# Optimization experiments

Hardware: AMD Instinct MI355X
Metric: run time of the kernel (lower is better)

## Reference

```python
import jax, jax.numpy as jnp
from jax import lax
import numpy as np

B, CIN, T, H, W = 32, 512, 16, 7, 7
A = 9                 # 3 scales x 3 ratios
STRIDE = 16.0
NMS_THRESH = 0.7      # cfg.TEST.RPN_NMS_THRESH
POST_NMS = 300        # cfg.TEST.RPN_POST_NMS_TOP_N


def _gen_anchors():
    # faithful port of generate_anchors(base_size=16, ratios=[0.5,1,2], scales=[4,8,16])
    base = 16.0
    ratios = np.array([0.5, 1.0, 2.0])
    scales = np.array([4.0, 8.0, 16.0])
    ctr = (base - 1.0) / 2.0
    size = base * base
    ws = np.round(np.sqrt(size / ratios))
    hs = np.round(ws * ratios)
    def mk(ws, hs, xc, yc):
        return np.stack([xc - 0.5 * (ws - 1), yc - 0.5 * (hs - 1),
                         xc + 0.5 * (ws - 1), yc + 0.5 * (hs - 1)], 1)
    ratio_anchors = mk(ws, hs, ctr, ctr)            # [3,4]
    outs = []
    for a in ratio_anchors:                         # scale enum per ratio anchor
        w = a[2] - a[0] + 1.0
        h = a[3] - a[1] + 1.0
        xc = a[0] + 0.5 * (w - 1)
        yc = a[1] + 0.5 * (h - 1)
        outs.append(mk(w * scales, h * scales, xc, yc))
    return np.concatenate(outs, 0).astype(np.float32)  # [9,4]


def _shifted_anchors():
    sx = (np.arange(W) * STRIDE).astype(np.float32)
    sy = (np.arange(H) * STRIDE).astype(np.float32)
    mx, my = np.meshgrid(sx, sy)                    # x fastest, matches HWA flatten
    shifts = np.stack([mx.ravel(), my.ravel(), mx.ravel(), my.ravel()], 1)  # [K,4]
    return (shifts[:, None, :] + _gen_anchors()[None, :, :]).reshape(-1, 4)  # [K*A,4]

_ALL_ANCHORS = jnp.asarray(_shifted_anchors())      # [441,4]


def conv3d(x, w, b, pad):
    y = lax.conv_general_dilated(x, w, (1, 1, 1),
                                 [(pad[0], pad[0]), (pad[1], pad[1]), (pad[2], pad[2])],
                                 dimension_numbers=('NCDHW', 'OIDHW', 'NCDHW'))
    return y + b[None, :, None, None, None]


def conv1x1(x, w, b):
    return jnp.einsum('bchw,oc->bohw', x, w[:, :, 0, 0]) + b[None, :, None, None]


def softmax_2way(score):
    # reshape(x,2) -> softmax over dim 1 -> reshape back (fg/bg pairwise softmax)
    b, c, h, w = score.shape
    s = score.reshape(b, 2, (c // 2) * h, w)
    return jax.nn.softmax(s, axis=1).reshape(b, c, h, w)


def bbox_decode(anchors, deltas):
    # anchors [N,4], deltas [B,N,4] -> boxes [B,N,4] (bbox_transform_inv)
    w = anchors[:, 2] - anchors[:, 0] + 1.0
    h = anchors[:, 3] - anchors[:, 1] + 1.0
    cx = anchors[:, 0] + 0.5 * w
    cy = anchors[:, 1] + 0.5 * h
    pcx = deltas[..., 0] * w + cx
    pcy = deltas[..., 1] * h + cy
    pw = jnp.exp(deltas[..., 2]) * w
    ph = jnp.exp(deltas[..., 3]) * h
    return jnp.stack([pcx - 0.5 * pw, pcy - 0.5 * ph,
                      pcx + 0.5 * pw, pcy + 0.5 * ph], axis=-1)


def clip_boxes(boxes, info):
    # boxes [N,4], info = (im_h, im_w, scale)
    x1 = jnp.clip(boxes[:, 0], 0.0, info[1] - 1.0)
    y1 = jnp.clip(boxes[:, 1], 0.0, info[0] - 1.0)
    x2 = jnp.clip(boxes[:, 2], 0.0, info[1] - 1.0)
    y2 = jnp.clip(boxes[:, 3], 0.0, info[0] - 1.0)
    return jnp.stack([x1, y1, x2, y2], 1)


def nms_single(boxes, scores):
    # greedy NMS, fixed shapes: boxes [N,4] -> kept boxes padded to [POST_NMS,4]
    order = jnp.argsort(-scores)
    b = boxes[order]
    n = b.shape[0]
    areas = (b[:, 2] - b[:, 0] + 1.0) * (b[:, 3] - b[:, 1] + 1.0)
    idx = jnp.arange(n)
    def body(i, keep):
        xx1 = jnp.maximum(b[i, 0], b[:, 0])
        yy1 = jnp.maximum(b[i, 1], b[:, 1])
        xx2 = jnp.minimum(b[i, 2], b[:, 2])
        yy2 = jnp.minimum(b[i, 3], b[:, 3])
        inter = jnp.clip(xx2 - xx1 + 1.0, 0.0) * jnp.clip(yy2 - yy1 + 1.0, 0.0)
        iou = inter / (areas[i] + areas - inter)
        sup = (idx > i) & (iou > NMS_THRESH) & keep[i]
        return keep & ~sup
    keep = lax.fori_loop(0, n, body, jnp.ones((n,), bool))
    sel = jnp.sort(jnp.where(keep, idx, n))[:POST_NMS]
    valid = sel < n
    selc = jnp.minimum(sel, n - 1)
    return jnp.where(valid[:, None], b[selc], 0.0)


def proposal_layer(cls_prob, bbox_pred, im_info):
    b = cls_prob.shape[0]
    scores = cls_prob[:, A:, :, :].transpose(0, 2, 3, 1).reshape(b, -1)   # fg scores [B,K*A]
    deltas = bbox_pred.transpose(0, 2, 3, 1).reshape(b, -1, 4)
    props = bbox_decode(_ALL_ANCHORS, deltas)
    props = jax.vmap(clip_boxes)(props, im_info)
    boxes = jax.vmap(nms_single)(props, scores)                           # [B,POST_NMS,4]
    bidx = jnp.broadcast_to(jnp.arange(b, dtype=boxes.dtype)[:, None, None],
                            (b, POST_NMS, 1))
    return jnp.concatenate([bidx, boxes], axis=2)                         # [B,POST_NMS,5]


def setup_inputs() -> dict:
    key = jax.random.key(0)
    ks = jax.random.split(key, 8)
    s = 0.05
    return {
        'base_feat': jax.random.normal(ks[0], (B, CIN, T, H, W), jnp.float32),
        'im_info': jnp.tile(jnp.array([[112.0, 112.0, 1.0]], jnp.float32), (B, 1)),
        'gt_boxes': jnp.zeros((B, 1, 7), jnp.float32),
        'num_boxes': jnp.zeros((B,), jnp.int32),
        'rpn_conv_w': jax.random.normal(ks[1], (512, CIN, 3, 3, 3), jnp.float32) * s,
        'rpn_conv_b': jnp.zeros((512,), jnp.float32),
        't16_w': jax.random.normal(ks[2], (512, 512, 16, 3, 3), jnp.float32) * s,
        't16_b': jnp.zeros((512,), jnp.float32),
        'cls_w': jax.random.normal(ks[3], (2 * A, 512, 1, 1), jnp.float32) * s,
        'cls_b': jnp.zeros((2 * A,), jnp.float32),
        'bbox_w': jax.random.normal(ks[4], (4 * A, 512, 1, 1), jnp.float32) * s,
        'bbox_b': jnp.zeros((4 * A,), jnp.float32),
    }


def reference(base_feat, im_info, gt_boxes, num_boxes,
              rpn_conv_w, rpn_conv_b, t16_w, t16_b,
              cls_w, cls_b, bbox_w, bbox_b):
    x = jax.nn.relu(conv3d(base_feat, rpn_conv_w, rpn_conv_b, (1, 1, 1)))     # [B,512,16,7,7]
    f16 = jax.nn.relu(conv3d(x, t16_w, t16_b, (0, 1, 1)))                     # [B,512,1,7,7]
    f16 = f16.transpose(0, 2, 1, 3, 4).reshape(-1, 512, H, W)                 # [B,512,7,7]
    cls_score = conv1x1(f16, cls_w, cls_b)                                    # [B,18,7,7]
    cls_prob = softmax_2way(cls_score)
    bbox_pred = conv1x1(f16, bbox_w, bbox_b)                                  # [B,36,7,7]
    # proposals use .data in the original -> detached
    rois = proposal_layer(lax.stop_gradient(cls_prob),
                          lax.stop_gradient(bbox_pred), im_info)
    return rois, cls_prob, bbox_pred
```

## Files before the change

kernel.cpp:

```cpp
#include <hip/hip_runtime.h>
#include <hip/hip_bf16.h>
#include <cmath>

typedef __bf16 bf16_t;
typedef unsigned short u16;
typedef unsigned int u32;
typedef float f32x4 __attribute__((ext_vector_type(4)));
typedef short s16x8 __attribute__((ext_vector_type(8)));
typedef u32   u32x2 __attribute__((ext_vector_type(2)));
typedef u32   u32x4 __attribute__((ext_vector_type(4)));
#define DEVINL __device__ __forceinline__
#define POSTN 300

#define XPT_OFF  0ull
#define XP16_OFF 0ull
#define W1T_OFF  5971968ull
#define YTP_OFF  20127744ull
#define YT_OFF   23887872ull
#define F_OFF    45121536ull
#define PART_OFF 48332800ull
#define SC_OFF   51544064ull
#define BX_OFF   51600512ull
#define K1_OFF   51826304ull
#define K2_OFF   51881600ull
#define FLAG_OFF 52176512ull
#define NEED     52176516ull

DEVINL float ldf(const void* p, long i, int f32m) {
  return f32m ? ((const float*)p)[i] : (float)(((const bf16_t*)p)[i]);
}

DEVINL float clampf(float v, float lo, float hi) {
  if (!(v == v)) return lo;
  if (v < lo) return lo;
  if (v > hi) return hi;
  return v;
}

DEVINL void split3(float v, u16& hb, u16& mb, u16& lb) {
  bf16_t h = (bf16_t)v; float fh = (float)h;
  float r1 = v - fh;
  bf16_t m = (bf16_t)r1; float fm_ = (float)m;
  float r2 = r1 - fm_;
  bf16_t l = (bf16_t)r2;
  __builtin_memcpy(&hb, &h, 2);
  __builtin_memcpy(&mb, &m, 2);
  __builtin_memcpy(&lb, &l, 2);
}

__global__ __launch_bounds__(256) void detect_dtype(const void* bf, const void* w1, int* flag) {
  __shared__ int cnt;
  int tid = threadIdx.x;
  if (tid == 0) cnt = 0;
  __syncthreads();
  float a = (float)(((const bf16_t*)bf)[2 * tid]);
  float b = (float)(((const bf16_t*)w1)[2 * tid]);
  int wc = 0;
  if (!(a == a) || fabsf(a) > 1e20f || (a != 0.f && fabsf(a) < 1e-20f)) wc++;
  if (!(b == b) || fabsf(b) > 1e20f || (b != 0.f && fabsf(b) < 1e-20f)) wc++;
  atomicAdd(&cnt, wc);
  __syncthreads();
  if (tid == 0) *flag = (cnt >= 16) ? 1 : 0;
}

__global__ __launch_bounds__(256) void build_koff(int* k1, int* k2) {
  int i = blockIdx.x * 256 + threadIdx.x;
  if (i < 13824) {
    int ci = i / 27, tap = i % 27;
    k1[i] = ci * 1458 + (tap / 9) * 81 + ((tap % 9) / 3) * 9 + (tap % 3);
  }
  if (i < 73728) {
    int ci = i / 144, tap = i % 144;
    k2[i] = ci * 1296 + (tap / 9) * 81 + ((tap % 9) / 3) * 9 + (tap % 3);
  }
}

__global__ __launch_bounds__(256) void build_w1t(const void* __restrict__ w1,
                                                 u16* __restrict__ w1T,
                                                 const int* __restrict__ flagp) {
  if (*flagp != 0) return;
  int id = blockIdx.x * 256 + threadIdx.x;
  if (id >= 512 * 27 * 64) return;
  int co = id / 1728, r = id % 1728, tap = r / 64, cio = r % 64;
  const u16* W = (const u16*)w1;
  u16 t[8];
#pragma unroll
  for (int e = 0; e < 8; e++) t[e] = W[co * 13824 + (cio * 8 + e) * 27 + tap];
  u32x4 v = { (u32)t[0] | ((u32)t[1] << 16), (u32)t[2] | ((u32)t[3] << 16),
              (u32)t[4] | ((u32)t[5] << 16), (u32)t[6] | ((u32)t[7] << 16) };
  *(u32x4*)&w1T[co * 13824 + tap * 512 + cio * 8] = v;
}

__global__ __launch_bounds__(256) void pad_f32(const void* __restrict__ X,
                                               float* __restrict__ XpT,
                                               const int* __restrict__ flagp, int cb) {
  if (*flagp == 0) return;
  int e = blockIdx.x * 256 + threadIdx.x;
  if (e >= 4 * 512 * 1458) return;
  int bc = e / 1458, p = e % 1458;
  int tp = p / 81, hp = (p % 81) / 9, wp = p % 9;
  float v = 0.f;
  if (tp >= 1 && tp < 17 && hp >= 1 && hp < 8 && wp >= 1 && wp < 8) {
    int f = (tp - 1) * 49 + (hp - 1) * 7 + (wp - 1);
    v = ((const float*)X)[((long)cb * 512 + bc) * 784 + f];
  }
  XpT[e] = v;
}

__global__ __launch_bounds__(256) void pad_b16(const void* __restrict__ X,
                                               u16* __restrict__ Xp16,
                                               const int* __restrict__ flagp, int cb) {
  if (*flagp != 0) return;
  int id = blockIdx.x * 256 + threadIdx.x;
  if (id >= 5832 * 64) return;
  int pos = id >> 6, cio = id & 63;
  int b = pos / 1458, r = pos % 1458;
  int tp = r / 81, hp = (r % 81) / 9, wp = r % 9;
  u16 t[8] = {0, 0, 0, 0, 0, 0, 0, 0};
  if (tp >= 1 && tp < 17 && hp >= 1 && hp < 8 && wp >= 1 && wp < 8) {
    int f = (tp - 1) * 49 + (hp - 1) * 7 + (wp - 1);
    const u16* Xs = (const u16*)X;
#pragma unroll
    for (int e = 0; e < 8; e++)
      t[e] = Xs[((long)(cb + b) * 512 + cio * 8 + e) * 784 + f];
  }
  u32x4 v = { (u32)t[0] | ((u32)t[1] << 16), (u32)t[2] | ((u32)t[3] << 16),
              (u32)t[4] | ((u32)t[5] << 16), (u32)t[6] | ((u32)t[7] << 16) };
  *(u32x4*)&Xp16[(long)pos * 512 + cio * 8] = v;
}

template <int MODE>
__global__ __launch_bounds__(256) void gemm_f32(
    const float* __restrict__ Act, const void* __restrict__ Wgt, const void* __restrict__ bias,
    float* __restrict__ Yt, float* __restrict__ Part,
    const int* __restrict__ koff, const int* __restrict__ flagp) {
  const int f32m = *flagp;
  if (f32m == 0) return;
  const int tid = threadIdx.x;
  int mt, nt, s = 0;
  if (MODE == 1) { mt = blockIdx.x % 49; nt = blockIdx.x / 49; }
  else           { mt = blockIdx.x & 3;  nt = (blockIdx.x >> 2) & 7; s = blockIdx.x >> 5; }
  const int m0 = mt * 64, n0 = nt * 64;
  const int K     = (MODE == 1) ? 13824 : 9216;
  const int kBase = (MODE == 1) ? 0     : s * 9216;
  const int WROW  = (MODE == 1) ? 13824 : 73728;
  const int MTOT  = (MODE == 1) ? 3136  : 196;

  __shared__ __align__(16) float As[64][68];
  __shared__ __align__(16) float Bs[64][68];

  const int am = tid & 63, akq = tid >> 6;
  long aBase;
  {
    int m = m0 + am; if (m > MTOT - 1) m = MTOT - 1;
    if (MODE == 1) {
      int b = m / 784, r = m % 784, t = r / 49, h = (r % 49) / 7, w = r % 7;
      aBase = (long)b * (512 * 1458) + t * 81 + h * 9 + w;
    } else {
      int b = m / 49, r = m % 49, h = r / 7, w = r % 7;
      aBase = (long)b * (512 * 1296) + h * 9 + w;
    }
  }
  const int bn = tid >> 2, bks = (tid & 3) * 16;
  const long bBase = (long)(n0 + bn) * WROW + kBase;

  float acc[4][4] = {{0.f}};
  const int tx = tid & 15, ty = tid >> 4;

  for (int k0 = 0; k0 < K; k0 += 64) {
    __syncthreads();
#pragma unroll
    for (int j = 0; j < 16; j++) {
      int kk = akq * 16 + j;
      As[kk][am] = Act[aBase + koff[kBase + k0 + kk]];
    }
#pragma unroll
    for (int j = 0; j < 16; j++) {
      int kk = bks + j;
      Bs[kk][bn] = ldf(Wgt, bBase + k0 + kk, f32m);
    }
    __syncthreads();
#pragma unroll 8
    for (int k = 0; k < 64; k++) {
      f32x4 a = *(const f32x4*)&As[k][tx * 4];
      f32x4 b = *(const f32x4*)&Bs[k][ty * 4];
#pragma unroll
      for (int i = 0; i < 4; i++)
#pragma unroll
        for (int j = 0; j < 4; j++) acc[i][j] += a[i] * b[j];
    }
  }

#pragma unroll
  for (int i = 0; i < 4; i++) {
    int m = m0 + tx * 4 + i;
#pragma unroll
    for (int j = 0; j < 4; j++) {
      int n = n0 + ty * 4 + j;
      if (MODE == 1) {
        int b = m / 784, r = m % 784, t = r / 49, h = (r % 49) / 7, w = r % 7;
        float v = acc[i][j] + ldf(bias, n, f32m);
        v = fmaxf(v, 0.f);
        Yt[(long)(b * 512 + n) * 1296 + t * 81 + (h + 1) * 9 + (w + 1)] = v;
      } else {
        if (m < 196) Part[((long)s * 196 + m) * 512 + n] = acc[i][j];
      }
    }
  }
}

__global__ __launch_bounds__(256) void gemm_mf1(
    const u16* __restrict__ Xp16, const u16* __restrict__ w1T, const void* __restrict__ bias,
    u32x2* __restrict__ YtP, const int* __restrict__ flagp) {
  if (*flagp != 0) return;
  const int tid = threadIdx.x;
  const int mt = blockIdx.x % 25, nt = blockIdx.x / 25;
  const int m0 = mt * 128, n0 = nt * 64;

  __shared__ u16 As[128 * 64];
  __shared__ u16 Bs[64 * 64];

  int rowbase[4];
#pragma unroll
  for (int i = 0; i < 4; ++i) {
    int id = tid + 256 * i;
    int m = m0 + (id >> 3); if (m > 3135) m = 3135;
    int b = m / 784, r = m % 784, t = r / 49, h = (r % 49) / 7, w = r % 7;
    rowbase[i] = ((((b * 18) + (t + 1)) * 9 + (h + 1)) * 9 + (w + 1)) * 512;
  }
  const int bn = tid & 63, bq = tid >> 6;
  const u16* __restrict__ Bp = w1T + (long)(n0 + bn) * 13824;
  const int bwb = bn * 64, bsw = (bn & 7) << 3;

  const int lane = tid & 63, wv = tid >> 6;
  const int wm = (wv & 1) * 64, wn = (wv >> 1) * 32;
  const int lr = lane & 15, lq = lane >> 4;

  f32x4 acc[4][2];
#pragma unroll
  for (int i = 0; i < 4; ++i)
#pragma unroll
    for (int j = 0; j < 2; ++j) acc[i][j] = f32x4{0.f, 0.f, 0.f, 0.f};

  for (int tap = 0; tap < 27; ++tap) {
    const int dt = tap / 9, dh = (tap % 9) / 3, dw = tap % 3;
    const int tapshift = dt * 41472 + dh * 4608 + dw * 512;
    for (int cib = 0; cib < 8; ++cib) {
      const int off = tapshift + cib * 64;
      __syncthreads();
      u32x4 va[4];
#pragma unroll
      for (int i = 0; i < 4; ++i) {
        int id = tid + 256 * i;
        va[i] = *(const u32x4*)&Xp16[rowbase[i] + off + (id & 7) * 8];
      }
#pragma unroll
      for (int i = 0; i < 4; ++i) {
        int id = tid + 256 * i;
        int row = id >> 3, oct = id & 7;
        *(u32x4*)&As[row * 64 + ((oct * 8) ^ ((row & 7) << 3))] = va[i];
      }
      {
        const u32x4* wp = (const u32x4*)(Bp + tap * 512 + cib * 64 + bq * 16);
        *(u32x4*)&Bs[bwb + ((bq * 16) ^ bsw)] = wp[0];
        *(u32x4*)&Bs[bwb + ((bq * 16 + 8) ^ bsw)] = wp[1];
      }
      __syncthreads();
#pragma unroll
      for (int kk = 0; kk < 64; kk += 32) {
        const int kf = kk + lq * 8;
        s16x8 a[4], b[2];
#pragma unroll
        for (int fm = 0; fm < 4; ++fm) {
          const int row = wm + fm * 16 + lr;
          a[fm] = *(const s16x8*)&As[row * 64 + (kf ^ ((lr & 7) << 3))];
        }
#pragma unroll
        for (int fn = 0; fn < 2; ++fn) {
          const int row = wn + fn * 16 + lr;
          b[fn] = *(const s16x8*)&Bs[row * 64 + (kf ^ ((lr & 7) << 3))];
        }
#pragma unroll
        for (int fm = 0; fm < 4; ++fm)
#pragma unroll
          for (int fn = 0; fn < 2; ++fn)
            acc[fm][fn] = __builtin_amdgcn_mfma_f32_16x16x32_bf16(a[fm], b[fn], acc[fm][fn], 0, 0, 0);
      }
    }
  }

#pragma unroll
  for (int fn = 0; fn < 2; ++fn) {
    const int n = n0 + wn + fn * 16 + lr;
    const float bv = (float)(((const bf16_t*)bias)[n]);
#pragma unroll
    for (int fm = 0; fm < 4; ++fm)
#pragma unroll
      for (int r = 0; r < 4; ++r) {
        const int m = m0 + wm + fm * 16 + lq * 4 + r;
        if (m < 3136) {
          int b = m / 784, rr = m % 784, t = rr / 49, hh = (rr % 49) / 7, ww = rr % 7;
          float v = fmaxf(acc[fm][fn][r] + bv, 0.f);
          u16 hb, mb, lb; split3(v, hb, mb, lb);
          long idx = (long)(b * 512 + n) * 1296 + t * 81 + (hh + 1) * 9 + (ww + 1);
          YtP[idx] = u32x2{ ((u32)hb << 16) | mb, (u32)lb };
        }
      }
  }
}

__global__ __launch_bounds__(256) void gemm_mf2(
    const u32x2* __restrict__ AP, const void* __restrict__ Wgt,
    float* __restrict__ Part, const int* __restrict__ koff, const int* __restrict__ flagp) {
  if (*flagp != 0) return;
  const int tid = threadIdx.x;
  const int mt = blockIdx.x & 3, nt = (blockIdx.x >> 2) & 7, s = blockIdx.x >> 5;
  const int m0 = mt * 64, n0 = nt * 64;
  const int kBase = s * 9216;

  __shared__ u16 AsH[64 * 64], AsM[64 * 64], AsL[64 * 64];
  __shared__ u16 Bs[64 * 64];

  const int am = tid & 63, kq = tid >> 6;
  long aBase;
  {
    int m = m0 + am; if (m > 195) m = 195;
    int b = m / 49, r = m % 49, h = r / 7, w = r % 7;
    aBase = (long)b * (512 * 1296) + h * 9 + w;
  }
  const u32x2* __restrict__ Ap = AP + aBase;
  const int awb = am * 64, asw = (am & 7) << 3;

  const int bn = tid & 63, bq = tid >> 6;
  const u16* __restrict__ Bp = (const u16*)Wgt + (long)(n0 + bn) * 73728 + kBase;
  const int bwb = bn * 64, bsw = (bn & 7) << 3;

  const int lane = tid & 63, wv = tid >> 6;
  const int wm = (wv & 1) * 32, wn = (wv >> 1) * 32;
  const int lr = lane & 15, lq = lane >> 4;

  f32x4 acc[2][2];
#pragma unroll
  for (int i = 0; i < 2; ++i)
#pragma unroll
    for (int j = 0; j < 2; ++j) acc[i][j] = f32x4{0.f, 0.f, 0.f, 0.f};

  for (int k0 = 0; k0 < 9216; k0 += 64) {
    __syncthreads();
#pragma unroll
    for (int g = 0; g < 2; ++g) {
      const int o = kBase + k0 + kq * 16 + g * 8;
      const int i0 = koff[o + 0], i1 = koff[o + 1], i2 = koff[o + 2], i3 = koff[o + 3],
                i4 = koff[o + 4], i5 = koff[o + 5], i6 = koff[o + 6], i7 = koff[o + 7];
      const u32x2 q0 = Ap[i0], q1 = Ap[i1], q2 = Ap[i2], q3 = Ap[i3],
                  q4 = Ap[i4], q5 = Ap[i5], q6 = Ap[i6], q7 = Ap[i7];
      const int wi = awb + ((kq * 16 + g * 8) ^ asw);
      u32x4 H = { (q0.x >> 16) | (q1.x & 0xffff0000u), (q2.x >> 16) | (q3.x & 0xffff0000u),
                  (q4.x >> 16) | (q5.x & 0xffff0000u), (q6.x >> 16) | (q7.x & 0xffff0000u) };
      *(u32x4*)&AsH[wi] = H;
      u32x4 M = { (q0.x & 0xffffu) | (q1.x << 16), (q2.x & 0xffffu) | (q3.x << 16),
                  (q4.x & 0xffffu) | (q5.x << 16), (q6.x & 0xffffu) | (q7.x << 16) };
      *(u32x4*)&AsM[wi] = M;
      u32x4 L = { q0.y | (q1.y << 16), q2.y | (q3.y << 16),
                  q4.y | (q5.y << 16), q6.y | (q7.y << 16) };
      *(u32x4*)&AsL[wi] = L;
    }
    {
      const u32x4* wp = (const u32x4*)(Bp + k0 + bq * 16);
      *(u32x4*)&Bs[bwb + ((bq * 16) ^ bsw)] = wp[0];
      *(u32x4*)&Bs[bwb + ((bq * 16 + 8) ^ bsw)] = wp[1];
    }
    __syncthreads();
#pragma unroll
    for (int kk = 0; kk < 64; kk += 32) {
      const int kf = kk + lq * 8;
      s16x8 ah[2], am_[2], al[2], b[2];
#pragma unroll
      for (int fm = 0; fm < 2; ++fm) {
        const int off = (wm + fm * 16 + lr) * 64 + (kf ^ ((lr & 7) << 3));
        ah[fm] = *(const s16x8*)&AsH[off];
        am_[fm] = *(const s16x8*)&AsM[off];
        al[fm] = *(const s16x8*)&AsL[off];
      }
#pragma unroll
      for (int fn = 0; fn < 2; ++fn) {
        const int off = (wn + fn * 16 + lr) * 64 + (kf ^ ((lr & 7) << 3));
        b[fn] = *(const s16x8*)&Bs[off];
      }
#pragma unroll
      for (int fm = 0; fm < 2; ++fm)
#pragma unroll
        for (int fn = 0; fn < 2; ++fn) {
          acc[fm][fn] = __builtin_amdgcn_mfma_f32_16x16x32_bf16(ah[fm], b[fn], acc[fm][fn], 0, 0, 0);
          acc[fm][fn] = __builtin_amdgcn_mfma_f32_16x16x32_bf16(am_[fm], b[fn], acc[fm][fn], 0, 0, 0);
          acc[fm][fn] = __builtin_amdgcn_mfma_f32_16x16x32_bf16(al[fm], b[fn], acc[fm][fn], 0, 0, 0);
        }
    }
  }

#pragma unroll
  for (int fn = 0; fn < 2; ++fn) {
    const int n = n0 + wn + fn * 16 + lr;
#pragma unroll
    for (int fm = 0; fm < 2; ++fm)
#pragma unroll
      for (int r = 0; r < 4; ++r) {
        const int m = m0 + wm + fm * 16 + lq * 4 + r;
        if (m < 196) Part[((long)s * 196 + m) * 512 + n] = acc[fm][fn][r];
      }
  }
}

__global__ __launch_bounds__(256) void reduce2(const float* __restrict__ Part,
                                               const void* __restrict__ bias,
                                               float* __restrict__ F,
                                               const int* __restrict__ flagp, int chunk) {
  int f32m = *flagp;
  int idx = blockIdx.x * 256 + threadIdx.x;
  if (idx >= 196 * 512) return;
  int m = idx >> 9, n = idx & 511;
  float v = 0.f;
#pragma unroll
  for (int s = 0; s < 8; s++) v += Part[((long)s * 196 + m) * 512 + n];
  v += ldf(bias, n, f32m);
  F[((long)chunk * 196 + m) * 512 + n] = fmaxf(v, 0.f);
}

__global__ __launch_bounds__(256) void heads(
    const float* __restrict__ F, const void* __restrict__ cls_w, const void* __restrict__ cls_b,
    const void* __restrict__ bbox_w, const void* __restrict__ bbox_b,
    const void* __restrict__ im_info, float* __restrict__ out_cls, float* __restrict__ out_bbox,
    float* __restrict__ scores, float* __restrict__ boxes, const int* __restrict__ flagp) {
  int f32m = *flagp;
  int m = blockIdx.x;
  int bg = m / 49, r2 = m % 49, h = r2 / 7, w = r2 % 7;
  __shared__ float Fr[512];
  __shared__ float partial[256];
  __shared__ float outv[54];
  int tid = threadIdx.x;
  Fr[tid] = F[(long)m * 512 + tid];
  Fr[tid + 256] = F[(long)m * 512 + tid + 256];
  __syncthreads();
  int o = tid & 63, ch = tid >> 6;
  float p = 0.f;
  if (o < 54) {
    const void* wp = (o < 18) ? cls_w : bbox_w;
    long wrow = (o < 18) ? (long)o * 512 : (long)(o - 18) * 512;
    int c0 = ch * 128;
    for (int c = c0; c < c0 + 128; c++) p += Fr[c] * ldf(wp, wrow + c, f32m);
  }
  partial[tid] = p;
  __syncthreads();
  if (tid < 54) {
    float v = partial[tid] + partial[tid + 64] + partial[tid + 128] + partial[tid + 192];
    v += (tid < 18) ? ldf(cls_b, tid, f32m) : ldf(bbox_b, tid - 18, f32m);
    outv[tid] = v;
  }
  __syncthreads();
  if (tid < 18) {
    int a = tid % 9;
    float s0 = outv[a], s1 = outv[a + 9];
    float mx = fmaxf(s0, s1);
    float e0 = expf(s0 - mx), e1 = expf(s1 - mx);
    float pr = ((tid < 9) ? e0 : e1) / (e0 + e1);
    if (!(pr == pr)) pr = 0.f;
    out_cls[(((long)(bg * 18 + tid)) * 7 + h) * 7 + w] = pr;
    if (tid >= 9) scores[bg * 441 + (h * 7 + w) * 9 + a] = pr;
  } else if (tid < 54) {
    float v = outv[tid];
    if (!(v == v)) v = 0.f;
    out_bbox[(((long)(bg * 36 + (tid - 18))) * 7 + h) * 7 + w] = v;
  } else if (tid < 63) {
    int a = tid - 54;
    int ridx = a / 3, sidx = a % 3;
    float ratio = (ridx == 0) ? 0.5f : ((ridx == 1) ? 1.f : 2.f);
    float scale = (sidx == 0) ? 4.f : ((sidx == 1) ? 8.f : 16.f);
    float ws0 = rintf(sqrtf(256.f / ratio));
    float hs0 = rintf(ws0 * ratio);
    float x1 = 7.5f - 0.5f * (ws0 - 1.f), y1 = 7.5f - 0.5f * (hs0 - 1.f);
    float x2 = 7.5f + 0.5f * (ws0 - 1.f), y2 = 7.5f + 0.5f * (hs0 - 1.f);
    float w_ = x2 - x1 + 1.f, h_ = y2 - y1 + 1.f;
    float xc = x1 + 0.5f * (w_ - 1.f), yc = y1 + 0.5f * (h_ - 1.f);
    float ws2 = w_ * scale, hs2 = h_ * scale;
    float ax1 = xc - 0.5f * (ws2 - 1.f) + w * 16.f;
    float ay1 = yc - 0.5f * (hs2 - 1.f) + h * 16.f;
    float ax2 = xc + 0.5f * (ws2 - 1.f) + w * 16.f;
    float ay2 = yc + 0.5f * (hs2 - 1.f) + h * 16.f;
    float wA = ax2 - ax1 + 1.f, hA = ay2 - ay1 + 1.f;
    float cxA = ax1 + 0.5f * wA, cyA = ay1 + 0.5f * hA;
    float d0 = outv[18 + 4 * a], d1 = outv[19 + 4 * a];
    float d2 = outv[20 + 4 * a], d3 = outv[21 + 4 * a];
    float pcx = d0 * wA + cxA, pcy = d1 * hA + cyA;
    float pw = expf(d2) * wA, ph = expf(d3) * hA;
    float iw = ldf(im_info, bg * 3 + 1, f32m) - 1.f;
    float ih = ldf(im_info, bg * 3 + 0, f32m) - 1.f;
    float bx1 = clampf(pcx - 0.5f * pw, 0.f, iw);
    float by1 = clampf(pcy - 0.5f * ph, 0.f, ih);
    float bx2 = clampf(pcx + 0.5f * pw, 0.f, iw);
    float by2 = clampf(pcy + 0.5f * ph, 0.f, ih);
    int ai = bg * 441 + (h * 7 + w) * 9 + a;
    boxes[ai * 4 + 0] = bx1; boxes[ai * 4 + 1] = by1;
    boxes[ai * 4 + 2] = bx2; boxes[ai * 4 + 3] = by2;
  }
}

__global__ __launch_bounds__(256) void nms_kernel(const float* __restrict__ scores,
                                                  const float* __restrict__ boxes,
                                                  float* __restrict__ rois) {
  int bg = blockIdx.x;
  int tid = threadIdx.x;
  __shared__ float rsc[441];
  __shared__ unsigned short ord[441];
  __shared__ float sbx[441][4];
  __shared__ float sar[441];
  __shared__ unsigned long long sup[441][8];
  __shared__ unsigned long long kw[8];
  for (int i = tid; i < 441; i += 256) { rsc[i] = scores[bg * 441 + i]; ord[i] = (unsigned short)i; }
  if (tid < 8) kw[tid] = 0ull;
  __syncthreads();
  for (int i = tid; i < 441; i += 256) {
    float si = rsc[i];
    int rk = 0;
    for (int j = 0; j < 441; j++) {
      float sj = rsc[j];
      rk += (sj > si) || (sj == si && j < i);
    }
    if (rk < 441) ord[rk] = (unsigned short)i;
  }
  __syncthreads();
  for (int r = tid; r < 441; r += 256) {
    int i = ord[r];
    float x1 = boxes[(bg * 441 + i) * 4 + 0], y1 = boxes[(bg * 441 + i) * 4 + 1];
    float x2 = boxes[(bg * 441 + i) * 4 + 2], y2 = boxes[(bg * 441 + i) * 4 + 3];
    sbx[r][0] = x1; sbx[r][1] = y1; sbx[r][2] = x2; sbx[r][3] = y2;
    sar[r] = (x2 - x1 + 1.f) * (y2 - y1 + 1.f);
  }
  __syncthreads();
  for (int task = tid; task < 441 * 7; task += 256) {
    int r = task / 7, wd = task % 7;
    float x1 = sbx[r][0], y1 = sbx[r][1], x2 = sbx[r][2], y2 = sbx[r][3];
    float ar = sar[r];
    unsigned long long msk = 0ull;
    int jbase = wd * 64;
    for (int bit = 0; bit < 64; bit++) {
      int j = jbase + bit;
      if (j > r && j < 441) {
        float xx1 = fmaxf(x1, sbx[j][0]);
        float yy1 = fmaxf(y1, sbx[j][1]);
        float xx2 = fminf(x2, sbx[j][2]);
        float yy2 = fminf(y2, sbx[j][3]);
        float iwv = fmaxf(xx2 - xx1 + 1.f, 0.f);
        float ihv = fmaxf(yy2 - yy1 + 1.f, 0.f);
        float inter = iwv * ihv;
        float iou = inter / (ar + sar[j] - inter);
        if (iou > 0.7f) msk |= (1ull << bit);
      }
    }
    sup[r][wd] = msk;
  }
  __syncthreads();
  if (tid < 64) {
    int wd = (tid < 7) ? tid : 7;
    unsigned long long rmw = 0ull;
    for (int i = 0; i < 441; i++) {
      int ow = i >> 6, obit = i & 63;
      int mykeep = ((rmw >> obit) & 1ull) ? 0 : 1;
      int kept = __shfl(mykeep, ow, 64);
      if (kept && wd < 7) rmw |= sup[i][wd];
    }
    if (wd < 7) {
      unsigned long long k = ~rmw;
      if (wd == 6) k &= (1ull << 57) - 1;
      kw[wd] = k;
    }
  }
  __syncthreads();
  for (int r = tid; r < POSTN; r += 256) {
    long oo = ((long)bg * POSTN + r) * 5;
    rois[oo] = (float)bg;
    rois[oo + 1] = 0.f; rois[oo + 2] = 0.f;
    rois[oo + 3] = 0.f; rois[oo + 4] = 0.f;
  }
  __syncthreads();
  for (int r = tid; r < 441; r += 256) {
    int wd = r >> 6, bit = r & 63;
    if ((kw[wd] >> bit) & 1ull) {
      int slot = 0;
      for (int q = 0; q < wd; q++) slot += __popcll(kw[q]);
      slot += __popcll(kw[wd] & ((1ull << bit) - 1ull));
      if (slot < POSTN) {
        long oo = ((long)bg * POSTN + slot) * 5;
        rois[oo + 1] = sbx[r][0];
        rois[oo + 2] = sbx[r][1];
        rois[oo + 3] = sbx[r][2];
        rois[oo + 4] = sbx[r][3];
      }
    }
  }
}

__global__ __launch_bounds__(256) void scrub_f32(float* __restrict__ o, int n) {
  int i = blockIdx.x * 256 + threadIdx.x;
  if (i >= n) return;
  float v = o[i];
  if (!(v == v) || fabsf(v) > 1e30f) o[i] = 0.f;
}

__global__ __launch_bounds__(256) void fallback_out(float* __restrict__ out, int total) {
  int i = blockIdx.x * 256 + threadIdx.x;
  if (i >= total) return;
  out[i] = 0.f;
}

extern "C" void kernel_launch(void* const* d_in, const int* in_sizes, int n_in,
                              void* d_out, int out_size, void* d_ws, size_t ws_size,
                              hipStream_t stream) {
  const void* base_feat = d_in[0];
  const void* im_info   = d_in[1];
  const void* w1 = d_in[4];
  const void* b1 = d_in[5];
  const void* w2 = d_in[6];
  const void* b2 = d_in[7];
  const void* cw = d_in[8];
  const void* cb = d_in[9];
  const void* bw = d_in[10];
  const void* bb = d_in[11];
  float* out = (float*)d_out;

  if (ws_size < NEED) {
    fallback_out<<<(out_size + 255) / 256, 256, 0, stream>>>(out, out_size);
    return;
  }

  char* ws = (char*)d_ws;
  float* XpT  = (float*)(ws + XPT_OFF);
  u16*   Xp16 = (u16*)(ws + XP16_OFF);
  u16*   W1T  = (u16*)(ws + W1T_OFF);
  u32x2* YtP  = (u32x2*)(ws + YTP_OFF);
  float* Yt   = (float*)(ws + YT_OFF);
  float* F    = (float*)(ws + F_OFF);
  float* Part = (float*)(ws + PART_OFF);
  float* Sc   = (float*)(ws + SC_OFF);
  float* Bx   = (float*)(ws + BX_OFF);
  int*   K1   = (int*)(ws + K1_OFF);
  int*   K2   = (int*)(ws + K2_OFF);
  int*   Flag = (int*)(ws + FLAG_OFF);

  detect_dtype<<<1, 256, 0, stream>>>(base_feat, w1, Flag);
  build_koff<<<288, 256, 0, stream>>>(K1, K2);
  build_w1t<<<3456, 256, 0, stream>>>(w1, W1T, Flag);
  hipMemsetAsync(ws + YTP_OFF, 0, 45121536ull - YTP_OFF, stream);

  for (int c = 0; c < 8; c++) {
    pad_f32<<<11664, 256, 0, stream>>>(base_feat, XpT, Flag, c * 4);
    pad_b16<<<1458, 256, 0, stream>>>(base_feat, Xp16, Flag, c * 4);
    gemm_f32<1><<<392, 256, 0, stream>>>(XpT, w1, b1, Yt, nullptr, K1, Flag);
    gemm_mf1<<<200, 256, 0, stream>>>(Xp16, W1T, b1, YtP, Flag);
    gemm_f32<2><<<256, 256, 0, stream>>>(Yt, w2, nullptr, nullptr, Part, K2, Flag);
    gemm_mf2<<<256, 256, 0, stream>>>(YtP, w2, Part, K2, Flag);
    reduce2<<<392, 256, 0, stream>>>(Part, b2, F, Flag, c);
  }

  heads<<<1568, 256, 0, stream>>>(F, cw, cb, bw, bb, im_info,
                                  out + 48000, out + 76224, Sc, Bx, Flag);
  nms_kernel<<<32, 256, 0, stream>>>(Sc, Bx, out);
  scrub_f32<<<(out_size + 255) / 256, 256, 0, stream>>>(out, out_size);
}
```

Baseline: 11.56 ms.

## Retile conv GEMMs for more blocks and separate fp32/bf16 chunk loops

The bf16 path's first conv GEMM now uses 64x64 tiles, doubling its block count to 392. The second GEMM's split-K grows from 8 to 12 slices (384 blocks), with its partials placed in the freed Xp16 region and summed by a dedicated reduce. The fp32 path is split into its own loop over 4 chunks of 8 batches with matching grid changes, so the dead-path kernels for the other dtype are no longer launched on every iteration. The aim is better CU occupancy and fewer no-op launches, at the cost of more partial-sum traffic and less per-block reuse in the first GEMM.

```diff
diff --git a/kernel.cpp b/kernel.cpp
--- a/kernel.cpp
+++ b/kernel.cpp
@@ -95,9 +95,9 @@
                                                float* __restrict__ XpT,
                                                const int* __restrict__ flagp, int cb) {
   if (*flagp == 0) return;
-  int e = blockIdx.x * 256 + threadIdx.x;
-  if (e >= 4 * 512 * 1458) return;
-  int bc = e / 1458, p = e % 1458;
+  long e = (long)blockIdx.x * 256 + threadIdx.x;
+  if (e >= 8L * 512 * 1458) return;
+  long bc = e / 1458; int p = (int)(e % 1458);
   int tp = p / 81, hp = (p % 81) / 9, wp = p % 9;
   float v = 0.f;
   if (tp >= 1 && tp < 17 && hp >= 1 && hp < 8 && wp >= 1 && wp < 8) {
@@ -138,13 +138,12 @@
   if (f32m == 0) return;
   const int tid = threadIdx.x;
   int mt, nt, s = 0;
-  if (MODE == 1) { mt = blockIdx.x % 49; nt = blockIdx.x / 49; }
-  else           { mt = blockIdx.x & 3;  nt = (blockIdx.x >> 2) & 7; s = blockIdx.x >> 5; }
+  if (MODE == 1) { mt = blockIdx.x % 98; nt = blockIdx.x / 98; }
+  else           { mt = blockIdx.x % 7;  nt = (blockIdx.x / 7) % 8; s = blockIdx.x / 56; }
   const int m0 = mt * 64, n0 = nt * 64;
-  const int K     = (MODE == 1) ? 13824 : 9216;
-  const int kBase = (MODE == 1) ? 0     : s * 9216;
+  const int K     = (MODE == 1) ? 13824 : 18432;
+  const int kBase = (MODE == 1) ? 0     : s * 18432;
   const int WROW  = (MODE == 1) ? 13824 : 73728;
-  const int MTOT  = (MODE == 1) ? 3136  : 196;
 
   __shared__ __align__(16) float As[64][68];
   __shared__ __align__(16) float Bs[64][68];
@@ -152,11 +151,12 @@
   const int am = tid & 63, akq = tid >> 6;
   long aBase;
   {
-    int m = m0 + am; if (m > MTOT - 1) m = MTOT - 1;
+    int m = m0 + am;
     if (MODE == 1) {
       int b = m / 784, r = m % 784, t = r / 49, h = (r % 49) / 7, w = r % 7;
       aBase = (long)b * (512 * 1458) + t * 81 + h * 9 + w;
     } else {
+      if (m > 391) m = 391;
       int b = m / 49, r = m % 49, h = r / 7, w = r % 7;
       aBase = (long)b * (512 * 1296) + h * 9 + w;
     }
@@ -203,7 +203,7 @@
         v = fmaxf(v, 0.f);
         Yt[(long)(b * 512 + n) * 1296 + t * 81 + (h + 1) * 9 + (w + 1)] = v;
       } else {
-        if (m < 196) Part[((long)s * 196 + m) * 512 + n] = acc[i][j];
+        if (m < 392) Part[((long)s * 392 + m) * 512 + n] = acc[i][j];
       }
     }
   }
@@ -214,31 +214,32 @@
     u32x2* __restrict__ YtP, const int* __restrict__ flagp) {
   if (*flagp != 0) return;
   const int tid = threadIdx.x;
-  const int mt = blockIdx.x % 25, nt = blockIdx.x / 25;
-  const int m0 = mt * 128, n0 = nt * 64;
-
-  __shared__ u16 As[128 * 64];
+  const int mt = blockIdx.x % 49, nt = blockIdx.x / 49;
+  const int m0 = mt * 64, n0 = nt * 64;
+
+  __shared__ u16 As[64 * 64];
   __shared__ u16 Bs[64 * 64];
 
-  int rowbase[4];
-#pragma unroll
-  for (int i = 0; i < 4; ++i) {
-    int id = tid + 256 * i;
-    int m = m0 + (id >> 3); if (m > 3135) m = 3135;
+  const int arow = tid >> 2, aq = tid & 3;
+  int rowbase;
+  {
+    int m = m0 + arow;
     int b = m / 784, r = m % 784, t = r / 49, h = (r % 49) / 7, w = r % 7;
-    rowbase[i] = ((((b * 18) + (t + 1)) * 9 + (h + 1)) * 9 + (w + 1)) * 512;
-  }
+    rowbase = ((((b * 18) + (t + 1)) * 9 + (h + 1)) * 9 + (w + 1)) * 512;
+  }
+  const int awb = arow * 64, asw = (arow & 7) << 3;
+
   const int bn = tid & 63, bq = tid >> 6;
   const u16* __restrict__ Bp = w1T + (long)(n0 + bn) * 13824;
   const int bwb = bn * 64, bsw = (bn & 7) << 3;
 
   const int lane = tid & 63, wv = tid >> 6;
-  const int wm = (wv & 1) * 64, wn = (wv >> 1) * 32;
+  const int wm = (wv & 1) * 32, wn = (wv >> 1) * 32;
   const int lr = lane & 15, lq = lane >> 4;
 
-  f32x4 acc[4][2];
-#pragma unroll
-  for (int i = 0; i < 4; ++i)
+  f32x4 acc[2][2];
+#pragma unroll
+  for (int i = 0; i < 2; ++i)
 #pragma unroll
     for (int j = 0; j < 2; ++j) acc[i][j] = f32x4{0.f, 0.f, 0.f, 0.f};
 
@@ -248,18 +249,10 @@
     for (int cib = 0; cib < 8; ++cib) {
       const int off = tapshift + cib * 64;
       __syncthreads();
-      u32x4 va[4];
-#pragma unroll
-      for (int i = 0; i < 4; ++i) {
-        int id = tid + 256 * i;
-        va[i] = *(const u32x4*)&Xp16[rowbase[i] + off + (id & 7) * 8];
-      }
-#pragma unroll
-      for (int i = 0; i < 4; ++i) {
-        int id = tid + 256 * i;
-        int row = id >> 3, oct = id & 7;
-        *(u32x4*)&As[row * 64 + ((oct * 8) ^ ((row & 7) << 3))] = va[i];
-      }
+      u32x4 v0 = *(const u32x4*)&Xp16[rowbase + off + aq * 8];
+      u32x4 v1 = *(const u32x4*)&Xp16[rowbase + off + (aq + 4) * 8];
+      *(u32x4*)&As[awb + ((aq * 8) ^ asw)] = v0;
+      *(u32x4*)&As[awb + (((aq + 4) * 8) ^ asw)] = v1;
       {
         const u32x4* wp = (const u32x4*)(Bp + tap * 512 + cib * 64 + bq * 16);
         *(u32x4*)&Bs[bwb + ((bq * 16) ^ bsw)] = wp[0];
@@ -269,9 +262,9 @@
 #pragma unroll
       for (int kk = 0; kk < 64; kk += 32) {
         const int kf = kk + lq * 8;
-        s16x8 a[4], b[2];
-#pragma unroll
-        for (int fm = 0; fm < 4; ++fm) {
+        s16x8 a[2], b[2];
+#pragma unroll
+        for (int fm = 0; fm < 2; ++fm) {
           const int row = wm + fm * 16 + lr;
           a[fm] = *(const s16x8*)&As[row * 64 + (kf ^ ((lr & 7) << 3))];
         }
@@ -281,7 +274,7 @@
           b[fn] = *(const s16x8*)&Bs[row * 64 + (kf ^ ((lr & 7) << 3))];
         }
 #pragma unroll
-        for (int fm = 0; fm < 4; ++fm)
+        for (int fm = 0; fm < 2; ++fm)
 #pragma unroll
           for (int fn = 0; fn < 2; ++fn)
             acc[fm][fn] = __builtin_amdgcn_mfma_f32_16x16x32_bf16(a[fm], b[fn], acc[fm][fn], 0, 0, 0);
@@ -294,17 +287,15 @@
     const int n = n0 + wn + fn * 16 + lr;
     const float bv = (float)(((const bf16_t*)bias)[n]);
 #pragma unroll
-    for (int fm = 0; fm < 4; ++fm)
+    for (int fm = 0; fm < 2; ++fm)
 #pragma unroll
       for (int r = 0; r < 4; ++r) {
         const int m = m0 + wm + fm * 16 + lq * 4 + r;
-        if (m < 3136) {
-          int b = m / 784, rr = m % 784, t = rr / 49, hh = (rr % 49) / 7, ww = rr % 7;
-          float v = fmaxf(acc[fm][fn][r] + bv, 0.f);
-          u16 hb, mb, lb; split3(v, hb, mb, lb);
-          long idx = (long)(b * 512 + n) * 1296 + t * 81 + (hh + 1) * 9 + (ww + 1);
-          YtP[idx] = u32x2{ ((u32)hb << 16) | mb, (u32)lb };
-        }
+        int b = m / 784, rr = m % 784, t = rr / 49, hh = (rr % 49) / 7, ww = rr % 7;
+        float v = fmaxf(acc[fm][fn][r] + bv, 0.f);
+        u16 hb, mb, lb; split3(v, hb, mb, lb);
+        long idx = (long)(b * 512 + n) * 1296 + t * 81 + (hh + 1) * 9 + (ww + 1);
+        YtP[idx] = u32x2{ ((u32)hb << 16) | mb, (u32)lb };
       }
   }
 }
@@ -316,7 +307,7 @@
   const int tid = threadIdx.x;
   const int mt = blockIdx.x & 3, nt = (blockIdx.x >> 2) & 7, s = blockIdx.x >> 5;
   const int m0 = mt * 64, n0 = nt * 64;
-  const int kBase = s * 9216;
+  const int kBase = s * 6144;
 
   __shared__ u16 AsH[64 * 64], AsM[64 * 64], AsL[64 * 64];
   __shared__ u16 Bs[64 * 64];
@@ -345,7 +336,7 @@
 #pragma unroll
     for (int j = 0; j < 2; ++j) acc[i][j] = f32x4{0.f, 0.f, 0.f, 0.f};
 
-  for (int k0 = 0; k0 < 9216; k0 += 64) {
+  for (int k0 = 0; k0 < 6144; k0 += 64) {
     __syncthreads();
 #pragma unroll
     for (int g = 0; g < 2; ++g) {
@@ -411,19 +402,34 @@
   }
 }
 
-__global__ __launch_bounds__(256) void reduce2(const float* __restrict__ Part,
-                                               const void* __restrict__ bias,
-                                               float* __restrict__ F,
-                                               const int* __restrict__ flagp, int chunk) {
-  int f32m = *flagp;
+__global__ __launch_bounds__(256) void reduce2_f32(const float* __restrict__ Part,
+                                                   const void* __restrict__ bias,
+                                                   float* __restrict__ F,
+                                                   const int* __restrict__ flagp, int chunk) {
+  if (*flagp == 0) return;
+  int idx = blockIdx.x * 256 + threadIdx.x;
+  if (idx >= 392 * 512) return;
+  int m = idx >> 9, n = idx & 511;
+  float v = 0.f;
+#pragma unroll
+  for (int s = 0; s < 4; s++) v += Part[((long)s * 392 + m) * 512 + n];
+  v += ((const float*)bias)[n];
+  F[((long)(chunk * 392 + m)) * 512 + n] = fmaxf(v, 0.f);
+}
+
+__global__ __launch_bounds__(256) void reduce2_b16(const float* __restrict__ Part,
+                                                   const void* __restrict__ bias,
+                                                   float* __restrict__ F,
+                                                   const int* __restrict__ flagp, int chunk) {
+  if (*flagp != 0) return;
   int idx = blockIdx.x * 256 + threadIdx.x;
   if (idx >= 196 * 512) return;
   int m = idx >> 9, n = idx & 511;
   float v = 0.f;
 #pragma unroll
-  for (int s = 0; s < 8; s++) v += Part[((long)s * 196 + m) * 512 + n];
-  v += ldf(bias, n, f32m);
-  F[((long)chunk * 196 + m) * 512 + n] = fmaxf(v, 0.f);
+  for (int s = 0; s < 12; s++) v += Part[((long)s * 196 + m) * 512 + n];
+  v += (float)(((const bf16_t*)bias)[n]);
+  F[((long)(chunk * 196 + m)) * 512 + n] = fmaxf(v, 0.f);
 }
 
 __global__ __launch_bounds__(256) void heads(
@@ -633,32 +639,37 @@
   }
 
   char* ws = (char*)d_ws;
-  float* XpT  = (float*)(ws + XPT_OFF);
-  u16*   Xp16 = (u16*)(ws + XP16_OFF);
-  u16*   W1T  = (u16*)(ws + W1T_OFF);
-  u32x2* YtP  = (u32x2*)(ws + YTP_OFF);
-  float* Yt   = (float*)(ws + YT_OFF);
-  float* F    = (float*)(ws + F_OFF);
-  float* Part = (float*)(ws + PART_OFF);
-  float* Sc   = (float*)(ws + SC_OFF);
-  float* Bx   = (float*)(ws + BX_OFF);
-  int*   K1   = (int*)(ws + K1_OFF);
-  int*   K2   = (int*)(ws + K2_OFF);
-  int*   Flag = (int*)(ws + FLAG_OFF);
+  float* XpT   = (float*)(ws + XPT_OFF);
+  u16*   Xp16  = (u16*)(ws + XP16_OFF);
+  float* PartB = (float*)(ws + XP16_OFF);
+  u16*   W1T   = (u16*)(ws + W1T_OFF);
+  u32x2* YtP   = (u32x2*)(ws + YTP_OFF);
+  float* Yt    = (float*)(ws + YT_OFF);
+  float* F     = (float*)(ws + F_OFF);
+  float* PartF = (float*)(ws + PART_OFF);
+  float* Sc    = (float*)(ws + SC_OFF);
+  float* Bx    = (float*)(ws + BX_OFF);
+  int*   K1    = (int*)(ws + K1_OFF);
+  int*   K2    = (int*)(ws + K2_OFF);
+  int*   Flag  = (int*)(ws + FLAG_OFF);
 
   detect_dtype<<<1, 256, 0, stream>>>(base_feat, w1, Flag);
   build_koff<<<288, 256, 0, stream>>>(K1, K2);
   build_w1t<<<3456, 256, 0, stream>>>(w1, W1T, Flag);
   hipMemsetAsync(ws + YTP_OFF, 0, 45121536ull - YTP_OFF, stream);
 
+  for (int c = 0; c < 4; c++) {
+    pad_f32<<<23328, 256, 0, stream>>>(base_feat, XpT, Flag, c * 8);
+    gemm_f32<1><<<784, 256, 0, stream>>>(XpT, w1, b1, Yt, nullptr, K1, Flag);
+    gemm_f32<2><<<224, 256, 0, stream>>>(Yt, w2, nullptr, nullptr, PartF, K2, Flag);
+    reduce2_f32<<<784, 256, 0, stream>>>(PartF, b2, F, Flag, c);
+  }
+
   for (int c = 0; c < 8; c++) {
-    pad_f32<<<11664, 256, 0, stream>>>(base_feat, XpT, Flag, c * 4);
     pad_b16<<<1458, 256, 0, stream>>>(base_feat, Xp16, Flag, c * 4);
-    gemm_f32<1><<<392, 256, 0, stream>>>(XpT, w1, b1, Yt, nullptr, K1, Flag);
-    gemm_mf1<<<200, 256, 0, stream>>>(Xp16, W1T, b1, YtP, Flag);
-    gemm_f32<2><<<256, 256, 0, stream>>>(Yt, w2, nullptr, nullptr, Part, K2, Flag);
-    gemm_mf2<<<256, 256, 0, stream>>>(YtP, w2, Part, K2, Flag);
-    reduce2<<<392, 256, 0, stream>>>(Part, b2, F, Flag, c);
+    gemm_mf1<<<392, 256, 0, stream>>>(Xp16, W1T, b1, YtP, Flag);
+    gemm_mf2<<<384, 256, 0, stream>>>(YtP, w2, PartB, K2, Flag);
+    reduce2_b16<<<392, 256, 0, stream>>>(PartB, b2, F, Flag, c);
   }
 
   heads<<<1568, 256, 0, stream>>>(F, cw, cb, bw, bb, im_info,
```

Measured after the change: 10.32 ms. 1.12x faster.
